# Performance work log

Measured on AMD Instinct MI355X. Metric: run time of the kernel, lower is better.

The kernel has to match this reference:

```python
import jax, jax.numpy as jnp
import numpy as np

N_NODES = 50000


def _gcn_norm(edge_index, n):
    # Add self-loops (PyG GCNConv default) and compute symmetric normalization.
    src = jnp.concatenate([edge_index[0], jnp.arange(n, dtype=edge_index.dtype)])
    dst = jnp.concatenate([edge_index[1], jnp.arange(n, dtype=edge_index.dtype)])
    deg = jax.ops.segment_sum(jnp.ones(src.shape[0], dtype=jnp.float32), dst,
                              num_segments=n)
    dinv = jnp.where(deg > 0, jax.lax.rsqrt(deg), 0.0)
    norm = dinv[src] * dinv[dst]  # [E+N]
    return src, dst, norm


def _gcn_conv(x, src, dst, norm, W, b, n):
    h = x @ W                              # [N, out] linear transform first
    msgs = h[src] * norm[:, None]          # gather + edge-wise scale [E+N, out]
    out = jax.ops.segment_sum(msgs, dst, num_segments=n)  # scatter-add
    return out + b


def setup_inputs() -> dict:
    key = jax.random.key(0)
    k1, k2, k3, k4 = jax.random.split(key, 4)
    N, E, F, H, C = N_NODES, 1600000, 128, 128, 64
    x = jax.random.normal(k1, (N, F), dtype=jnp.float32)
    edge_index = jax.random.randint(k2, (2, E), 0, N, dtype=jnp.int64)
    W1 = jax.random.normal(k3, (F, H), dtype=jnp.float32) * 0.05
    b1 = jnp.zeros((H,), dtype=jnp.float32)
    W2 = jax.random.normal(k4, (H, C), dtype=jnp.float32) * 0.05
    b2 = jnp.zeros((C,), dtype=jnp.float32)
    return {"x": x, "edge_index": edge_index, "W1": W1, "b1": b1,
            "W2": W2, "b2": b2}


def reference(x, edge_index, W1, b1, W2, b2):
    n = x.shape[0]
    src, dst, norm = _gcn_norm(edge_index, n)
    h = _gcn_conv(x, src, dst, norm, W1, b1, n)
    h = jax.nn.relu(h)
    out = _gcn_conv(h, src, dst, norm, W2, b2, n)
    return out
```

## Files before the change

### kernel.cpp

```cpp
#include <hip/hip_runtime.h>
#include <hip/hip_bf16.h>
#include <stdint.h>

#define N_NODES 50000
#define N_EDGES 1600000
#define N_TOT   (N_EDGES + N_NODES)
#define NBKT      256
#define BKT_NODES 196
#define BKT_CAP   7168
#define TILE      4096
#define EPT       16
#define ZROW      N_NODES

typedef unsigned short u16;
typedef __attribute__((ext_vector_type(8))) short short8;
typedef __attribute__((ext_vector_type(4))) float floatx4;

__device__ __forceinline__ float b2f(u16 u) {
    union { unsigned int i; float f; } v; v.i = ((unsigned int)u) << 16; return v.f;
}
__device__ __forceinline__ float asf(unsigned u) {
    union { unsigned int i; float f; } v; v.i = u; return v.f;
}
__device__ __forceinline__ u16 f2b(float f) {
    union { unsigned int i; float f; } v; v.f = f;
    unsigned int r = (v.i + 0x7FFFu + ((v.i >> 16) & 1u)) >> 16;
    return (u16)r;
}

__global__ __launch_bounds__(256) void k_part(const int* __restrict__ ei,
                                              const unsigned* __restrict__ xw,
                                              int* __restrict__ flags,
                                              unsigned* __restrict__ pairs,
                                              int* __restrict__ bktcnt) {
    __shared__ unsigned pairsL[TILE];
    __shared__ unsigned char bktL[TILE];
    __shared__ int hist[NBKT], incl[NBKT], delta[NBKT];
    __shared__ int zc, pc;
    int tid = threadIdx.x;
    long base = (long)blockIdx.x * TILE;
    hist[tid] = 0;
    if (tid == 0) { zc = 0; pc = 0; }
    __syncthreads();
    unsigned hw = ((const unsigned*)ei)[2 * tid + 1];
    atomicAdd(&zc, hw == 0 ? 1 : 0);
    if (blockIdx.x == 0) {
        unsigned w = xw[tid];
        int ex = (w >> 7) & 0xFF;
        atomicAdd(&pc, ((ex == 0) || (ex >= 0x60 && ex <= 0x9F)) ? 1 : 0);
    }
    __syncthreads();
    int i64 = zc > 250;
    if (blockIdx.x == 0 && tid == 0) {
        flags[0] = (pc < 160) ? 1 : 0;
        flags[1] = i64;
    }

    int myb[EPT], myrank[EPT]; unsigned myp[EPT];
#pragma unroll
    for (int t = 0; t < EPT; t++) {
        long idx = base + t * 256 + tid;
        int b = -1; unsigned p = 0;
        if (idx < N_TOT) {
            int s, d;
            if (idx < N_EDGES) {
                if (i64) { s = ei[2 * idx]; d = ei[2 * (N_EDGES + idx)]; }
                else     { s = ei[idx];     d = ei[N_EDGES + idx]; }
            } else {
                s = d = (int)(idx - N_EDGES);
            }
            b = d / BKT_NODES;
            p = (unsigned)s | ((unsigned)(d - b * BKT_NODES) << 16);
        }
        myb[t] = b; myp[t] = p;
        myrank[t] = (b >= 0) ? atomicAdd(&hist[b], 1) : 0;
    }
    __syncthreads();

    int tot = hist[tid];
    incl[tid] = tot;
    __syncthreads();
    for (int o = 1; o < NBKT; o <<= 1) {
        int t2 = (tid >= o) ? incl[tid - o] : 0;
        __syncthreads();
        incl[tid] += t2;
        __syncthreads();
    }
    int excl = incl[tid] - tot;
    int gb = atomicAdd(&bktcnt[tid], tot);
    hist[tid]  = excl;
    delta[tid] = tid * BKT_CAP + gb - excl;
    __syncthreads();

#pragma unroll
    for (int t = 0; t < EPT; t++) {
        if (myb[t] >= 0) {
            int slot = hist[myb[t]] + myrank[t];
            pairsL[slot] = myp[t];
            bktL[slot]   = (unsigned char)myb[t];
        }
    }
    __syncthreads();
    int count = incl[NBKT - 1];
    for (int i = tid; i < count; i += 256) {
        int b = bktL[i];
        int pos = delta[b] + i;
        if (pos - b * BKT_CAP < BKT_CAP)
            pairs[pos] = pairsL[i];
    }
}

__global__ __launch_bounds__(256) void k_bucket(const unsigned* __restrict__ pairs,
                                                const int* __restrict__ bktcnt,
                                                int* __restrict__ rowstart,
                                                int* __restrict__ deg,
                                                float* __restrict__ dinv,
                                                u16* __restrict__ csr) {
    __shared__ u16 csrL[BKT_CAP];
    __shared__ int degL[NBKT], curL[NBKT], scanT[NBKT];
    int b = blockIdx.x, tid = threadIdx.x;
    int cv = bktcnt[tid];
    scanT[tid] = cv;
    __syncthreads();
    for (int o = 1; o < NBKT; o <<= 1) {
        int t = (tid >= o) ? scanT[tid - o] : 0;
        __syncthreads();
        scanT[tid] += t;
        __syncthreads();
    }
    int cnt  = bktcnt[b];
    int base = scanT[b] - cnt;
    __syncthreads();

    const unsigned* reg = pairs + (size_t)b * BKT_CAP;
    degL[tid] = 0;
    __syncthreads();
    for (int i = tid; i < cnt; i += 256)
        atomicAdd(&degL[reg[i] >> 16], 1);
    __syncthreads();
    int v = degL[tid];
    scanT[tid] = v;
    __syncthreads();
    for (int o = 1; o < NBKT; o <<= 1) {
        int t = (tid >= o) ? scanT[tid - o] : 0;
        __syncthreads();
        scanT[tid] += t;
        __syncthreads();
    }
    int excl = scanT[tid] - v;
    curL[tid] = excl;
    int n = b * BKT_NODES + tid;
    if (tid < BKT_NODES && n < N_NODES) {
        rowstart[n] = base + excl;
        deg[n]      = v;
        dinv[n]     = rsqrtf((float)v);
    }
    __syncthreads();
    for (int i = tid; i < cnt; i += 256) {
        unsigned p = reg[i];
        int slot = atomicAdd(&curL[p >> 16], 1);
        csrL[slot] = (u16)(p & 0xFFFFu);
    }
    __syncthreads();
    for (int i = tid; i < cnt; i += 256)
        csr[base + i] = csrL[i];
}

template<int NOUT, bool ADYN>
__global__ __launch_bounds__(256) void k_gemm(const void* __restrict__ A,
                                              const void* __restrict__ W,
                                              const float* __restrict__ dinv,
                                              u16* __restrict__ out, int M,
                                              const int* __restrict__ flags) {
    const int isf32 = flags[0];
    constexpr int LDW = 136;
    __shared__ __align__(16) u16 Wt[NOUT * LDW];
    int tid = threadIdx.x;
    if (blockIdx.x == 0 && tid < NOUT)
        out[(size_t)M * NOUT + tid] = 0;
    const float* Wf = (const float*)W;
    const u16*   Wu = (const u16*)W;
    for (int idx = tid; idx < 128 * NOUT; idx += 256) {
        int k = idx / NOUT, n = idx % NOUT;
        Wt[n * LDW + k] = isf32 ? f2b(Wf[idx]) : Wu[idx];
    }
    __syncthreads();

    int wave = tid >> 6, lane = tid & 63;
    int quad = lane >> 4, l16 = lane & 15;
    int r0 = blockIdx.x * 64 + wave * 16;
    int r = r0 + l16; if (r >= M) r = M - 1;

    floatx4 acc[NOUT / 16];
#pragma unroll
    for (int i = 0; i < NOUT / 16; i++) acc[i] = (floatx4)(0.f);

#pragma unroll
    for (int ks = 0; ks < 4; ks++) {
        short8 a;
        if (ADYN && isf32) {
            const float* af = (const float*)A + (size_t)r * 128 + ks * 32 + quad * 8;
            float4 v0 = ((const float4*)af)[0];
            float4 v1 = ((const float4*)af)[1];
            a[0] = (short)f2b(v0.x); a[1] = (short)f2b(v0.y);
            a[2] = (short)f2b(v0.z); a[3] = (short)f2b(v0.w);
            a[4] = (short)f2b(v1.x); a[5] = (short)f2b(v1.y);
            a[6] = (short)f2b(v1.z); a[7] = (short)f2b(v1.w);
        } else {
            a = ((const short8*)((const u16*)A + (size_t)r * 128))[ks * 4 + quad];
        }
#pragma unroll
        for (int nt = 0; nt < NOUT / 16; nt++) {
            const short8* bp = (const short8*)&Wt[(nt * 16 + l16) * LDW + ks * 32 + quad * 8];
            acc[nt] = __builtin_amdgcn_mfma_f32_16x16x32_bf16(a, *bp, acc[nt], 0, 0, 0);
        }
    }
    float sc[4];
#pragma unroll
    for (int j = 0; j < 4; j++) {
        int row = r0 + quad * 4 + j;
        sc[j] = dinv[row < M ? row : 0];
    }
#pragma unroll
    for (int nt = 0; nt < NOUT / 16; nt++) {
#pragma unroll
        for (int j = 0; j < 4; j++) {
            int row = r0 + quad * 4 + j;
            if (row < M)
                out[(size_t)row * NOUT + nt * 16 + l16] = f2b(acc[nt][j] * sc[j]);
        }
    }
}

#define ACCU(u, j) { acc[j].x += asf((u) << 16); acc[j].y += asf((u) & 0xFFFF0000u); }
#define ACC4(q)    { ACCU(q.x,0) ACCU(q.y,1) ACCU(q.z,2) ACCU(q.w,3) }

__global__ __launch_bounds__(256) void k_agg1(const u16* __restrict__ h,
                                              const u16* __restrict__ csr,
                                              const int* __restrict__ rowstart,
                                              const int* __restrict__ deg,
                                              const float* __restrict__ dinv,
                                              const void* __restrict__ bias,
                                              u16* __restrict__ out,
                                              const int* __restrict__ flags) {
    int wave = threadIdx.x >> 6, lane = threadIdx.x & 63;
    int d = blockIdx.x * 4 + wave;
    int grp = lane >> 4, l16 = lane & 15;
    int start = rowstart[d], dg = deg[d], end = start + dg;
    int rounds = (dg + 3) >> 2;
    const uint4* hb = (const uint4*)h;
    float2 acc[4];
#pragma unroll
    for (int j = 0; j < 4; j++) acc[j] = make_float2(0.f, 0.f);

    int e0 = start + grp;
    int s;
    uint4 q0, q1, q2, q3;
    s = (e0      < end) ? csr[e0]      : ZROW; q0 = hb[(size_t)s * 16 + l16];
    s = (e0 + 4  < end) ? csr[e0 + 4]  : ZROW; q1 = hb[(size_t)s * 16 + l16];
    s = (e0 + 8  < end) ? csr[e0 + 8]  : ZROW; q2 = hb[(size_t)s * 16 + l16];
    s = (e0 + 12 < end) ? csr[e0 + 12] : ZROW; q3 = hb[(size_t)s * 16 + l16];
    int r = 4;
    for (; r + 3 < rounds; r += 4) {
        int e = e0 + 4 * r;
        ACC4(q0) s = (e      < end) ? csr[e]      : ZROW; q0 = hb[(size_t)s * 16 + l16];
        ACC4(q1) s = (e + 4  < end) ? csr[e + 4]  : ZROW; q1 = hb[(size_t)s * 16 + l16];
        ACC4(q2) s = (e + 8  < end) ? csr[e + 8]  : ZROW; q2 = hb[(size_t)s * 16 + l16];
        ACC4(q3) s = (e + 12 < end) ? csr[e + 12] : ZROW; q3 = hb[(size_t)s * 16 + l16];
    }
    for (; r < rounds; r++) {
        int e = e0 + 4 * r;
        ACC4(q0) s = (e < end) ? csr[e] : ZROW;
        q0 = q1; q1 = q2; q2 = q3; q3 = hb[(size_t)s * 16 + l16];
    }
    ACC4(q0) ACC4(q1) ACC4(q2) ACC4(q3)
#pragma unroll
    for (int j = 0; j < 4; j++) {
        acc[j].x += __shfl_xor(acc[j].x, 16); acc[j].y += __shfl_xor(acc[j].y, 16);
        acc[j].x += __shfl_xor(acc[j].x, 32); acc[j].y += __shfl_xor(acc[j].y, 32);
    }
    if (grp == 0) {
        int isf32 = flags[0];
        float dd = dinv[d];
        u16 r8[8];
#pragma unroll
        for (int j = 0; j < 4; j++) {
            float bx = isf32 ? ((const float*)bias)[l16 * 8 + 2 * j]
                             : b2f(((const u16*)bias)[l16 * 8 + 2 * j]);
            float by = isf32 ? ((const float*)bias)[l16 * 8 + 2 * j + 1]
                             : b2f(((const u16*)bias)[l16 * 8 + 2 * j + 1]);
            float vx = acc[j].x * dd + bx;
            float vy = acc[j].y * dd + by;
            r8[2 * j]     = f2b(vx > 0.f ? vx : 0.f);
            r8[2 * j + 1] = f2b(vy > 0.f ? vy : 0.f);
        }
        uint4 o;
        o.x = r8[0] | ((unsigned)r8[1] << 16); o.y = r8[2] | ((unsigned)r8[3] << 16);
        o.z = r8[4] | ((unsigned)r8[5] << 16); o.w = r8[6] | ((unsigned)r8[7] << 16);
        ((uint4*)(out + (size_t)d * 128))[l16] = o;
    }
}

__global__ __launch_bounds__(256) void k_agg2(const u16* __restrict__ h,
                                              const u16* __restrict__ csr,
                                              const int* __restrict__ rowstart,
                                              const int* __restrict__ deg,
                                              const float* __restrict__ dinv,
                                              const void* __restrict__ bias,
                                              float* __restrict__ out,
                                              const int* __restrict__ flags) {
    int wave = threadIdx.x >> 6, lane = threadIdx.x & 63;
    int d = blockIdx.x * 4 + wave;
    int oct = lane >> 3, l8 = lane & 7;
    int start = rowstart[d], dg = deg[d], end = start + dg;
    int rounds = (dg + 7) >> 3;
    const uint4* hb = (const uint4*)h;
    float2 acc[4];
#pragma unroll
    for (int j = 0; j < 4; j++) acc[j] = make_float2(0.f, 0.f);

    int e0 = start + oct;
    int s;
    uint4 q0, q1, q2;
    s = (e0      < end) ? csr[e0]      : ZROW; q0 = hb[(size_t)s * 8 + l8];
    s = (e0 + 8  < end) ? csr[e0 + 8]  : ZROW; q1 = hb[(size_t)s * 8 + l8];
    s = (e0 + 16 < end) ? csr[e0 + 16] : ZROW; q2 = hb[(size_t)s * 8 + l8];
    int r = 3;
    for (; r + 2 < rounds; r += 3) {
        int e = e0 + 8 * r;
        ACC4(q0) s = (e      < end) ? csr[e]      : ZROW; q0 = hb[(size_t)s * 8 + l8];
        ACC4(q1) s = (e + 8  < end) ? csr[e + 8]  : ZROW; q1 = hb[(size_t)s * 8 + l8];
        ACC4(q2) s = (e + 16 < end) ? csr[e + 16] : ZROW; q2 = hb[(size_t)s * 8 + l8];
    }
    for (; r < rounds; r++) {
        int e = e0 + 8 * r;
        ACC4(q0) s = (e < end) ? csr[e] : ZROW;
        q0 = q1; q1 = q2; q2 = hb[(size_t)s * 8 + l8];
    }
    ACC4(q0) ACC4(q1) ACC4(q2)
#pragma unroll
    for (int j = 0; j < 4; j++) {
        acc[j].x += __shfl_xor(acc[j].x, 8);  acc[j].y += __shfl_xor(acc[j].y, 8);
        acc[j].x += __shfl_xor(acc[j].x, 16); acc[j].y += __shfl_xor(acc[j].y, 16);
        acc[j].x += __shfl_xor(acc[j].x, 32); acc[j].y += __shfl_xor(acc[j].y, 32);
    }
    if (oct == 0) {
        int isf32 = flags[0];
        float dd = dinv[d];
        float r8[8];
#pragma unroll
        for (int j = 0; j < 4; j++) {
            float bx = isf32 ? ((const float*)bias)[l8 * 8 + 2 * j]
                             : b2f(((const u16*)bias)[l8 * 8 + 2 * j]);
            float by = isf32 ? ((const float*)bias)[l8 * 8 + 2 * j + 1]
                             : b2f(((const u16*)bias)[l8 * 8 + 2 * j + 1]);
            r8[2 * j]     = acc[j].x * dd + bx;
            r8[2 * j + 1] = acc[j].y * dd + by;
        }
        float4* op = (float4*)(out + (size_t)d * 64) + l8 * 2;
        op[0] = make_float4(r8[0], r8[1], r8[2], r8[3]);
        op[1] = make_float4(r8[4], r8[5], r8[6], r8[7]);
    }
}

extern "C" void kernel_launch(void* const* d_in, const int* in_sizes, int n_in,
                              void* d_out, int out_size, void* d_ws, size_t ws_size,
                              hipStream_t stream) {
    const void* x  = d_in[0];
    const int*  ei = (const int*)d_in[1];
    const void* W1 = d_in[2];
    const void* b1 = d_in[3];
    const void* W2 = d_in[4];
    const void* b2 = d_in[5];
    float* out = (float*)d_out;

    char* ws = (char*)d_ws;
    int*      flags    = (int*)(ws + 0);
    int*      bktcnt   = (int*)(ws + 1024);
    int*      deg      = (int*)(ws + 4096);
    int*      rowstart = (int*)(ws + 204800);
    float*    dinv     = (float*)(ws + 405504);
    unsigned* pairs    = (unsigned*)(ws + 606208);
    u16*      csr      = (u16*)(ws + 7946240);
    u16*      h1       = (u16*)(ws + 11247616);
    u16*      out1     = (u16*)(ws + 24048640);
    u16*      h2       = (u16*)(ws + 606208);

    hipMemsetAsync(bktcnt, 0, NBKT * sizeof(int), stream);
    k_part   <<<(N_TOT + TILE - 1) / TILE, 256, 0, stream>>>(ei, (const unsigned*)x,
                                                             flags, pairs, bktcnt);
    k_bucket <<<NBKT, 256, 0, stream>>>(pairs, bktcnt, rowstart, deg, dinv, csr);

    k_gemm<128, true> <<<(N_NODES + 63) / 64, 256, 0, stream>>>(x, W1, dinv, h1, N_NODES, flags);
    k_agg1<<<N_NODES / 4, 256, 0, stream>>>(h1, csr, rowstart, deg, dinv, b1, out1, flags);
    k_gemm<64, false> <<<(N_NODES + 63) / 64, 256, 0, stream>>>(out1, W2, dinv, h2, N_NODES, flags);
    k_agg2<<<N_NODES / 4, 256, 0, stream>>>(h2, csr, rowstart, deg, dinv, b2, out, flags);
}
```

Baseline: 246.8 us.

## Pad CSR rows to multiples of 16 and remove bounds checks in aggregation

```diff
diff --git a/kernel.cpp b/kernel.cpp
--- a/kernel.cpp
+++ b/kernel.cpp
@@ -8,6 +8,7 @@
 #define NBKT      256
 #define BKT_NODES 196
 #define BKT_CAP   7168
+#define PBKT_CAP  9216
 #define TILE      4096
 #define EPT       16
 #define ZROW      N_NODES
@@ -15,6 +16,7 @@
 typedef unsigned short u16;
 typedef __attribute__((ext_vector_type(8))) short short8;
 typedef __attribute__((ext_vector_type(4))) float floatx4;
+typedef __attribute__((ext_vector_type(2))) float f2;
 
 __device__ __forceinline__ float b2f(u16 u) {
     union { unsigned int i; float f; } v; v.i = ((unsigned int)u) << 16; return v.f;
@@ -26,6 +28,23 @@
     union { unsigned int i; float f; } v; v.f = f;
     unsigned int r = (v.i + 0x7FFFu + ((v.i >> 16) & 1u)) >> 16;
     return (u16)r;
+}
+
+__device__ __forceinline__ void accu(f2& a, unsigned u) {
+    f2 r; r.x = asf(u << 16); r.y = asf(u & 0xFFFF0000u);
+    a += r;
+}
+__device__ __forceinline__ void acc4u(f2* a, uint4 q) {
+    accu(a[0], q.x); accu(a[1], q.y); accu(a[2], q.z); accu(a[3], q.w);
+}
+__device__ __forceinline__ void acc2u(f2* a, uint2 q) {
+    accu(a[0], q.x); accu(a[1], q.y);
+}
+__device__ __forceinline__ uint4 g256(const char* hB, unsigned s, unsigned lb) {
+    return *(const uint4*)(hB + ((s << 8) + lb));
+}
+__device__ __forceinline__ uint2 g128(const char* hB, unsigned s, unsigned lb) {
+    return *(const uint2*)(hB + ((s << 7) + lb));
 }
 
 __global__ __launch_bounds__(256) void k_part(const int* __restrict__ ei,
@@ -116,11 +135,21 @@
                                                 int* __restrict__ deg,
                                                 float* __restrict__ dinv,
                                                 u16* __restrict__ csr) {
-    __shared__ u16 csrL[BKT_CAP];
+    __shared__ u16 csrL[PBKT_CAP];
     __shared__ int degL[NBKT], curL[NBKT], scanT[NBKT];
     int b = blockIdx.x, tid = threadIdx.x;
-    int cv = bktcnt[tid];
-    scanT[tid] = cv;
+    int cnt = bktcnt[b];
+    const unsigned* reg = pairs + (size_t)b * BKT_CAP;
+    degL[tid] = 0;
+    __syncthreads();
+    for (int i = tid; i < cnt; i += 256)
+        atomicAdd(&degL[reg[i] >> 16], 1);
+    __syncthreads();
+    int n = b * BKT_NODES + tid;
+    int valid = (tid < BKT_NODES) && (n < N_NODES);
+    int v = degL[tid];
+    int pv = valid ? ((v + 15) & ~15) : 0;
+    scanT[tid] = pv;
     __syncthreads();
     for (int o = 1; o < NBKT; o <<= 1) {
         int t = (tid >= o) ? scanT[tid - o] : 0;
@@ -128,42 +157,26 @@
         scanT[tid] += t;
         __syncthreads();
     }
-    int cnt  = bktcnt[b];
-    int base = scanT[b] - cnt;
-    __syncthreads();
-
-    const unsigned* reg = pairs + (size_t)b * BKT_CAP;
-    degL[tid] = 0;
-    __syncthreads();
-    for (int i = tid; i < cnt; i += 256)
-        atomicAdd(&degL[reg[i] >> 16], 1);
-    __syncthreads();
-    int v = degL[tid];
-    scanT[tid] = v;
-    __syncthreads();
-    for (int o = 1; o < NBKT; o <<= 1) {
-        int t = (tid >= o) ? scanT[tid - o] : 0;
-        __syncthreads();
-        scanT[tid] += t;
-        __syncthreads();
-    }
-    int excl = scanT[tid] - v;
-    curL[tid] = excl;
-    int n = b * BKT_NODES + tid;
-    if (tid < BKT_NODES && n < N_NODES) {
-        rowstart[n] = base + excl;
+    int pexcl = scanT[tid] - pv;
+    curL[tid] = pexcl;
+    if (valid) {
+        rowstart[n] = b * PBKT_CAP + pexcl;
         deg[n]      = v;
         dinv[n]     = rsqrtf((float)v);
     }
+    int pcnt = scanT[NBKT - 1];
+    if (pcnt > PBKT_CAP) pcnt = PBKT_CAP;
+    __syncthreads();
+    for (int i = tid; i < pcnt; i += 256) csrL[i] = (u16)ZROW;
     __syncthreads();
     for (int i = tid; i < cnt; i += 256) {
         unsigned p = reg[i];
         int slot = atomicAdd(&curL[p >> 16], 1);
-        csrL[slot] = (u16)(p & 0xFFFFu);
-    }
-    __syncthreads();
-    for (int i = tid; i < cnt; i += 256)
-        csr[base + i] = csrL[i];
+        if (slot < PBKT_CAP) csrL[slot] = (u16)(p & 0xFFFFu);
+    }
+    __syncthreads();
+    for (int i = tid; i < pcnt; i += 256)
+        csr[(size_t)b * PBKT_CAP + i] = csrL[i];
 }
 
 template<int NOUT, bool ADYN>
@@ -232,9 +245,6 @@
     }
 }
 
-#define ACCU(u, j) { acc[j].x += asf((u) << 16); acc[j].y += asf((u) & 0xFFFF0000u); }
-#define ACC4(q)    { ACCU(q.x,0) ACCU(q.y,1) ACCU(q.z,2) ACCU(q.w,3) }
-
 __global__ __launch_bounds__(256) void k_agg1(const u16* __restrict__ h,
                                               const u16* __restrict__ csr,
                                               const int* __restrict__ rowstart,
@@ -246,34 +256,27 @@
     int wave = threadIdx.x >> 6, lane = threadIdx.x & 63;
     int d = blockIdx.x * 4 + wave;
     int grp = lane >> 4, l16 = lane & 15;
-    int start = rowstart[d], dg = deg[d], end = start + dg;
-    int rounds = (dg + 3) >> 2;
-    const uint4* hb = (const uint4*)h;
-    float2 acc[4];
-#pragma unroll
-    for (int j = 0; j < 4; j++) acc[j] = make_float2(0.f, 0.f);
-
-    int e0 = start + grp;
-    int s;
-    uint4 q0, q1, q2, q3;
-    s = (e0      < end) ? csr[e0]      : ZROW; q0 = hb[(size_t)s * 16 + l16];
-    s = (e0 + 4  < end) ? csr[e0 + 4]  : ZROW; q1 = hb[(size_t)s * 16 + l16];
-    s = (e0 + 8  < end) ? csr[e0 + 8]  : ZROW; q2 = hb[(size_t)s * 16 + l16];
-    s = (e0 + 12 < end) ? csr[e0 + 12] : ZROW; q3 = hb[(size_t)s * 16 + l16];
-    int r = 4;
-    for (; r + 3 < rounds; r += 4) {
-        int e = e0 + 4 * r;
-        ACC4(q0) s = (e      < end) ? csr[e]      : ZROW; q0 = hb[(size_t)s * 16 + l16];
-        ACC4(q1) s = (e + 4  < end) ? csr[e + 4]  : ZROW; q1 = hb[(size_t)s * 16 + l16];
-        ACC4(q2) s = (e + 8  < end) ? csr[e + 8]  : ZROW; q2 = hb[(size_t)s * 16 + l16];
-        ACC4(q3) s = (e + 12 < end) ? csr[e + 12] : ZROW; q3 = hb[(size_t)s * 16 + l16];
-    }
-    for (; r < rounds; r++) {
-        int e = e0 + 4 * r;
-        ACC4(q0) s = (e < end) ? csr[e] : ZROW;
-        q0 = q1; q1 = q2; q2 = q3; q3 = hb[(size_t)s * 16 + l16];
-    }
-    ACC4(q0) ACC4(q1) ACC4(q2) ACC4(q3)
+    int start = rowstart[d], dg = deg[d];
+    int pdg = (dg + 15) & ~15;
+    int C = pdg >> 2;
+    const ushort4* cp = (const ushort4*)(csr + start + grp * C);
+    int nc = C >> 2;
+    const char* hB = (const char*)h;
+    unsigned lb = (unsigned)l16 << 4;
+
+    f2 acc[4] = {};
+    ushort4 c = cp[0];
+    uint4 q0 = g256(hB, c.x, lb), q1 = g256(hB, c.y, lb),
+          q2 = g256(hB, c.z, lb), q3 = g256(hB, c.w, lb);
+    for (int k = 1; k < nc; k++) {
+        ushort4 cn = cp[k];
+        acc4u(acc, q0); q0 = g256(hB, cn.x, lb);
+        acc4u(acc, q1); q1 = g256(hB, cn.y, lb);
+        acc4u(acc, q2); q2 = g256(hB, cn.z, lb);
+        acc4u(acc, q3); q3 = g256(hB, cn.w, lb);
+    }
+    acc4u(acc, q0); acc4u(acc, q1); acc4u(acc, q2); acc4u(acc, q3);
+
 #pragma unroll
     for (int j = 0; j < 4; j++) {
         acc[j].x += __shfl_xor(acc[j].x, 16); acc[j].y += __shfl_xor(acc[j].y, 16);
@@ -311,55 +314,47 @@
                                               const int* __restrict__ flags) {
     int wave = threadIdx.x >> 6, lane = threadIdx.x & 63;
     int d = blockIdx.x * 4 + wave;
-    int oct = lane >> 3, l8 = lane & 7;
-    int start = rowstart[d], dg = deg[d], end = start + dg;
-    int rounds = (dg + 7) >> 3;
-    const uint4* hb = (const uint4*)h;
-    float2 acc[4];
-#pragma unroll
-    for (int j = 0; j < 4; j++) acc[j] = make_float2(0.f, 0.f);
-
-    int e0 = start + oct;
-    int s;
-    uint4 q0, q1, q2;
-    s = (e0      < end) ? csr[e0]      : ZROW; q0 = hb[(size_t)s * 8 + l8];
-    s = (e0 + 8  < end) ? csr[e0 + 8]  : ZROW; q1 = hb[(size_t)s * 8 + l8];
-    s = (e0 + 16 < end) ? csr[e0 + 16] : ZROW; q2 = hb[(size_t)s * 8 + l8];
-    int r = 3;
-    for (; r + 2 < rounds; r += 3) {
-        int e = e0 + 8 * r;
-        ACC4(q0) s = (e      < end) ? csr[e]      : ZROW; q0 = hb[(size_t)s * 8 + l8];
-        ACC4(q1) s = (e + 8  < end) ? csr[e + 8]  : ZROW; q1 = hb[(size_t)s * 8 + l8];
-        ACC4(q2) s = (e + 16 < end) ? csr[e + 16] : ZROW; q2 = hb[(size_t)s * 8 + l8];
-    }
-    for (; r < rounds; r++) {
-        int e = e0 + 8 * r;
-        ACC4(q0) s = (e < end) ? csr[e] : ZROW;
-        q0 = q1; q1 = q2; q2 = hb[(size_t)s * 8 + l8];
-    }
-    ACC4(q0) ACC4(q1) ACC4(q2)
-#pragma unroll
-    for (int j = 0; j < 4; j++) {
-        acc[j].x += __shfl_xor(acc[j].x, 8);  acc[j].y += __shfl_xor(acc[j].y, 8);
+    int grp = lane >> 4, l16 = lane & 15;
+    int start = rowstart[d], dg = deg[d];
+    int pdg = (dg + 15) & ~15;
+    int C = pdg >> 2;
+    const ushort4* cp = (const ushort4*)(csr + start + grp * C);
+    int nc = C >> 2;
+    const char* hB = (const char*)h;
+    unsigned lb = (unsigned)l16 << 3;
+
+    f2 acc[2] = {};
+    ushort4 c = cp[0];
+    uint2 q0 = g128(hB, c.x, lb), q1 = g128(hB, c.y, lb),
+          q2 = g128(hB, c.z, lb), q3 = g128(hB, c.w, lb);
+    for (int k = 1; k < nc; k++) {
+        ushort4 cn = cp[k];
+        acc2u(acc, q0); q0 = g128(hB, cn.x, lb);
+        acc2u(acc, q1); q1 = g128(hB, cn.y, lb);
+        acc2u(acc, q2); q2 = g128(hB, cn.z, lb);
+        acc2u(acc, q3); q3 = g128(hB, cn.w, lb);
+    }
+    acc2u(acc, q0); acc2u(acc, q1); acc2u(acc, q2); acc2u(acc, q3);
+
+#pragma unroll
+    for (int j = 0; j < 2; j++) {
         acc[j].x += __shfl_xor(acc[j].x, 16); acc[j].y += __shfl_xor(acc[j].y, 16);
         acc[j].x += __shfl_xor(acc[j].x, 32); acc[j].y += __shfl_xor(acc[j].y, 32);
     }
-    if (oct == 0) {
+    if (grp == 0) {
         int isf32 = flags[0];
         float dd = dinv[d];
-        float r8[8];
-#pragma unroll
-        for (int j = 0; j < 4; j++) {
-            float bx = isf32 ? ((const float*)bias)[l8 * 8 + 2 * j]
-                             : b2f(((const u16*)bias)[l8 * 8 + 2 * j]);
-            float by = isf32 ? ((const float*)bias)[l8 * 8 + 2 * j + 1]
-                             : b2f(((const u16*)bias)[l8 * 8 + 2 * j + 1]);
-            r8[2 * j]     = acc[j].x * dd + bx;
-            r8[2 * j + 1] = acc[j].y * dd + by;
-        }
-        float4* op = (float4*)(out + (size_t)d * 64) + l8 * 2;
-        op[0] = make_float4(r8[0], r8[1], r8[2], r8[3]);
-        op[1] = make_float4(r8[4], r8[5], r8[6], r8[7]);
+        float r4[4];
+#pragma unroll
+        for (int j = 0; j < 2; j++) {
+            float bx = isf32 ? ((const float*)bias)[l16 * 4 + 2 * j]
+                             : b2f(((const u16*)bias)[l16 * 4 + 2 * j]);
+            float by = isf32 ? ((const float*)bias)[l16 * 4 + 2 * j + 1]
+                             : b2f(((const u16*)bias)[l16 * 4 + 2 * j + 1]);
+            r4[2 * j]     = acc[j].x * dd + bx;
+            r4[2 * j + 1] = acc[j].y * dd + by;
+        }
+        ((float4*)(out + (size_t)d * 64))[l16] = make_float4(r4[0], r4[1], r4[2], r4[3]);
     }
 }
 
@@ -380,11 +375,11 @@
     int*      deg      = (int*)(ws + 4096);
     int*      rowstart = (int*)(ws + 204800);
     float*    dinv     = (float*)(ws + 405504);
-    unsigned* pairs    = (unsigned*)(ws + 606208);
-    u16*      csr      = (u16*)(ws + 7946240);
-    u16*      h1       = (u16*)(ws + 11247616);
-    u16*      out1     = (u16*)(ws + 24048640);
-    u16*      h2       = (u16*)(ws + 606208);
+    u16*      csr      = (u16*)(ws + 606208);
+    unsigned* pairs    = (unsigned*)(ws + 5324800);
+    u16*      h1       = (u16*)(ws + 5324800);
+    u16*      out1     = (u16*)(ws + 18125056);
+    u16*      h2       = (u16*)(ws + 5324800);
 
     hipMemsetAsync(bktcnt, 0, NBKT * sizeof(int), stream);
     k_part   <<<(N_TOT + TILE - 1) / TILE, 256, 0, stream>>>(ei, (const unsigned*)x,
```

Result: faster. 240.8 us (-2.5%).
